# Performance work log

Hardware: AMD Instinct MI355X
Metric: run time of the kernel (lower is better)

## Reference

```python
import jax, jax.numpy as jnp
import numpy as np


def setup_inputs() -> dict:
    key = jax.random.key(0)
    ks = jax.random.split(key, 8)
    Na, Nb = 4096, 4096
    Fa, Fb, D = 512, 512, 128
    E = 131072  # avg degree 32
    x_a = jax.random.normal(ks[0], (Na, Fa), dtype=jnp.float32)
    x_b = jax.random.normal(ks[1], (Nb, Fb), dtype=jnp.float32)
    W_a = jax.random.normal(ks[2], (Fa, D), dtype=jnp.float32) / np.sqrt(Fa).astype(np.float32)
    b_a = jnp.zeros((D,), dtype=jnp.float32)
    W_b = jax.random.normal(ks[3], (Fb, D), dtype=jnp.float32) / np.sqrt(Fb).astype(np.float32)
    b_b = jnp.zeros((D,), dtype=jnp.float32)
    edge_index_ab = jax.random.randint(ks[4], (2, E), 0, Nb, dtype=jnp.int64)  # rows in [0,Na), cols in [0,Nb)
    edge_index_ba = jax.random.randint(ks[5], (2, E), 0, Na, dtype=jnp.int64)  # rows in [0,Nb), cols in [0,Na)
    return {"x_a": x_a, "x_b": x_b, "W_a": W_a, "b_a": b_a, "W_b": W_b, "b_b": b_b,
            "edge_index_ab": edge_index_ab, "edge_index_ba": edge_index_ba}


def reference(x_a, x_b, W_a, b_a, W_b, b_b, edge_index_ab, edge_index_ba):
    Na, Nb = x_a.shape[0], x_b.shape[0]
    dt = x_a.dtype
    # per-node-type feature projections (LATTE.feature_projection + relu activation)
    h_a = jax.nn.relu(x_a @ W_a + b_a)  # [Na, D]
    h_b = jax.nn.relu(x_b @ W_b + b_b)  # [Nb, D]
    # sparse adjacencies as dense scatters (edge values = 1.0, duplicates accumulate like coalesced SpGEMM)
    A = jnp.zeros((Na, Nb), dtype=dt).at[edge_index_ab[0], edge_index_ab[1]].add(1.0)
    B = jnp.zeros((Nb, Na), dtype=dt).at[edge_index_ba[0], edge_index_ba[1]].add(1.0)
    # adamic-adar degree normalization: deg_A = colcount(A), deg_B = rowcount(B), both over shared dim k=Nb
    deg_A = jnp.zeros((Nb,), dtype=dt).at[edge_index_ab[1]].add(1.0)
    deg_B = jnp.zeros((Nb,), dtype=dt).at[edge_index_ba[0]].add(1.0)
    deg = deg_A + deg_B
    d = jnp.where(deg > 0, 1.0 / jnp.maximum(deg, 1.0), 0.0)  # inf -> 0 as in original
    # out = A @ D @ B  (adamic-adar composed metapath adjacency)
    C = (A * d[None, :]) @ B  # [Na, Na]
    # metapath aggregation: 2nd-order (composed) path on h_a plus 1st-order neighbors of type b
    out = C @ h_a + A @ h_b  # [Na, D]
    return out
```

## Files before the change

kernel.cpp:

```cpp
#include <hip/hip_runtime.h>


#define D_FEAT 128
#define F_IN 512
#define BCAP 256
#define NROW 4096

using short8 = __attribute__((ext_vector_type(8))) short;
using ushort4v = __attribute__((ext_vector_type(4))) unsigned short;
using f32x4  = __attribute__((ext_vector_type(4))) float;

struct Params {
    const float* xa; const float* Wa; const float* ba;
    const float* xb; const float* Wb; const float* bb;
    const int* ab_row; const int* ab_col;
    const int* ba_row; const int* ba_col;
    short* WfA; short* WfB;
    unsigned short* ha_bf;
    float* hb;
    unsigned* u_bf;
    int* cnt_ab; int* cnt_ba; int* degc;
    unsigned short* buck_ab; unsigned short* buck_ba;
    float* out;
    int Eab; int Eba;
};

__device__ inline unsigned short f2bf(float f) {
    unsigned u = __builtin_bit_cast(unsigned, f);
    unsigned r = (u + 0x7FFFu + ((u >> 16) & 1u)) >> 16;
    return (unsigned short)r;
}
__device__ inline float bf2f(unsigned short s) {
    unsigned u = ((unsigned)s) << 16;
    return __builtin_bit_cast(float, u);
}

__global__ __launch_bounds__(256) void w_prep_k(Params P) {
    int g = blockIdx.x * 256 + threadIdx.x;
    for (int z = g; z < 3 * NROW; z += 16384) P.cnt_ab[z] = 0;
    const float* W = (g < 8192) ? P.Wa : P.Wb;
    short* Wf = (g < 8192) ? P.WfA : P.WfB;
    int i = g & 8191;
    int l = i & 63;
    int c = (i >> 6) & 7;
    int t = i >> 9;
    int col = c * 16 + (l & 15);
    int kbase = t * 32 + (l >> 4) * 8;
    short8 o;
#pragma unroll
    for (int e = 0; e < 8; ++e) o[e] = (short)f2bf(W[(size_t)(kbase + e) * D_FEAT + col]);
    *(short8*)(Wf + (size_t)i * 8) = o;
}

__global__ __launch_bounds__(256) void edges_gemm_k(Params P, int nblk_g) {
    int blk = blockIdx.x;
    if (blk >= nblk_g) {
        int base = (blk - nblk_g) * 512 + threadIdx.x;
#pragma unroll
        for (int q = 0; q < 2; ++q) {
            int g = base + q * 256;
            if (g < P.Eab) {
                int r = P.ab_row[g], c = P.ab_col[g];
                int p = atomicAdd(&P.cnt_ab[r], 1);
                if (p < BCAP) P.buck_ab[(size_t)r * BCAP + p] = (unsigned short)c;
                atomicAdd(&P.degc[c], 1);
            } else if (g < P.Eab + P.Eba) {
                int e = g - P.Eab;
                int r = P.ba_row[e], c = P.ba_col[e];
                int p = atomicAdd(&P.cnt_ba[r], 1);
                if (p < BCAP) P.buck_ba[(size_t)r * BCAP + p] = (unsigned short)c;
            }
        }
        return;
    }
    __shared__ float red[4][16][132];
    const int tid = threadIdx.x;
    const bool isA = (blk < 256);
    const float* x; const short* Wf; const float* bias;
    if (isA) { x = P.xa; Wf = P.WfA; bias = P.ba; }
    else { blk -= 256; x = P.xb; Wf = P.WfB; bias = P.bb; }
    const int row0 = blk * 16;
    const int w = tid >> 6;
    const int l = tid & 63;
    const int lr = l & 15;
    const int lk = l >> 4;

    f32x4 acc[8];
#pragma unroll
    for (int c = 0; c < 8; ++c) acc[c] = (f32x4){0.f, 0.f, 0.f, 0.f};

    const float* xrow = x + (size_t)(row0 + lr) * F_IN;
    float4 xf[8];
#pragma unroll
    for (int ks = 0; ks < 4; ++ks) {
        const int k0 = (w * 4 + ks) * 32 + lk * 8;
        xf[2 * ks]     = *(const float4*)(xrow + k0);
        xf[2 * ks + 1] = *(const float4*)(xrow + k0 + 4);
    }

#pragma unroll
    for (int ks = 0; ks < 4; ++ks) {
        const int t = w * 4 + ks;
        float4 xf0 = xf[2 * ks];
        float4 xf1 = xf[2 * ks + 1];
        short8 afr;
        afr[0] = (short)f2bf(xf0.x); afr[1] = (short)f2bf(xf0.y);
        afr[2] = (short)f2bf(xf0.z); afr[3] = (short)f2bf(xf0.w);
        afr[4] = (short)f2bf(xf1.x); afr[5] = (short)f2bf(xf1.y);
        afr[6] = (short)f2bf(xf1.z); afr[7] = (short)f2bf(xf1.w);
        const short8* wfp = (const short8*)Wf + ((size_t)t * 8 * 64 + l);
#pragma unroll
        for (int c = 0; c < 8; ++c) {
            short8 bfr = wfp[c * 64];
            acc[c] = __builtin_amdgcn_mfma_f32_16x16x32_bf16(afr, bfr, acc[c], 0, 0, 0);
        }
    }

#pragma unroll
    for (int c = 0; c < 8; ++c)
#pragma unroll
        for (int r = 0; r < 4; ++r)
            red[w][lk * 4 + r][c * 16 + lr] = acc[c][r];
    __syncthreads();

#pragma unroll
    for (int q = 0; q < 2; ++q) {
        int fi = tid * 2 + q;
        int r = fi >> 5;
        int c4 = fi & 31;
        float4 s0 = *(const float4*)&red[0][r][c4 * 4];
        float4 s1 = *(const float4*)&red[1][r][c4 * 4];
        float4 s2 = *(const float4*)&red[2][r][c4 * 4];
        float4 s3 = *(const float4*)&red[3][r][c4 * 4];
        float4 bv = ((const float4*)bias)[c4];
        float ox = fmaxf(s0.x + s1.x + s2.x + s3.x + bv.x, 0.0f);
        float oy = fmaxf(s0.y + s1.y + s2.y + s3.y + bv.y, 0.0f);
        float oz = fmaxf(s0.z + s1.z + s2.z + s3.z + bv.z, 0.0f);
        float ow = fmaxf(s0.w + s1.w + s2.w + s3.w + bv.w, 0.0f);
        if (isA) {
            ushort4v ob;
            ob[0] = f2bf(ox); ob[1] = f2bf(oy); ob[2] = f2bf(oz); ob[3] = f2bf(ow);
            *(ushort4v*)(P.ha_bf + (size_t)(row0 + r) * D_FEAT + c4 * 4) = ob;
        } else {
            float4 o; o.x = ox; o.y = oy; o.z = oz; o.w = ow;
            ((float4*)(P.hb + (size_t)(row0 + r) * D_FEAT))[c4] = o;
        }
    }
}

#define GATHER8(CBASE)                                                        \
    {                                                                         \
        int c0 = cols[CBASE],     c1 = cols[CBASE + 1];                       \
        int c2 = cols[CBASE + 2], c3 = cols[CBASE + 3];                       \
        int c4 = cols[CBASE + 4], c5 = cols[CBASE + 5];                       \
        int c6 = cols[CBASE + 6], c7 = cols[CBASE + 7];                       \
        unsigned v0 = s2[(size_t)c0 * 64 + lane];                             \
        unsigned v1 = s2[(size_t)c1 * 64 + lane];                             \
        unsigned v2 = s2[(size_t)c2 * 64 + lane];                             \
        unsigned v3 = s2[(size_t)c3 * 64 + lane];                             \
        unsigned v4 = s2[(size_t)c4 * 64 + lane];                             \
        unsigned v5 = s2[(size_t)c5 * 64 + lane];                             \
        unsigned v6 = s2[(size_t)c6 * 64 + lane];                             \
        unsigned v7 = s2[(size_t)c7 * 64 + lane];                             \
        ax += (bf2f((unsigned short)v0) + bf2f((unsigned short)v1)) +         \
              (bf2f((unsigned short)v2) + bf2f((unsigned short)v3)) +         \
              ((bf2f((unsigned short)v4) + bf2f((unsigned short)v5)) +        \
               (bf2f((unsigned short)v6) + bf2f((unsigned short)v7)));        \
        ay += (bf2f((unsigned short)(v0 >> 16)) + bf2f((unsigned short)(v1 >> 16))) + \
              (bf2f((unsigned short)(v2 >> 16)) + bf2f((unsigned short)(v3 >> 16))) + \
              ((bf2f((unsigned short)(v4 >> 16)) + bf2f((unsigned short)(v5 >> 16))) + \
               (bf2f((unsigned short)(v6 >> 16)) + bf2f((unsigned short)(v7 >> 16)))); \
    }

__global__ __launch_bounds__(256) void gather_u_k(Params P) {
    int r = blockIdx.x * 4 + (threadIdx.x >> 6);
    if (r >= NROW) return;
    int lane = threadIdx.x & 63;
    int ncb = P.cnt_ba[r];
    int dgc = P.degc[r];
    float2 hbv = ((const float2*)P.hb)[(size_t)r * 64 + lane];
    int n = ncb > BCAP ? BCAP : ncb;
    const unsigned short* cols = P.buck_ba + (size_t)r * BCAP;
    const unsigned* s2 = (const unsigned*)P.ha_bf;
    float ax = 0.0f, ay = 0.0f;
    int e = 0;
    for (; e + 15 < n; e += 16) { GATHER8(e) GATHER8(e + 8) }
    for (; e + 3 < n; e += 4) {
        int c0 = cols[e], c1 = cols[e + 1], c2 = cols[e + 2], c3 = cols[e + 3];
        unsigned v0 = s2[(size_t)c0 * 64 + lane];
        unsigned v1 = s2[(size_t)c1 * 64 + lane];
        unsigned v2 = s2[(size_t)c2 * 64 + lane];
        unsigned v3 = s2[(size_t)c3 * 64 + lane];
        ax += (bf2f((unsigned short)v0) + bf2f((unsigned short)v1)) +
              (bf2f((unsigned short)v2) + bf2f((unsigned short)v3));
        ay += (bf2f((unsigned short)(v0 >> 16)) + bf2f((unsigned short)(v1 >> 16))) +
              (bf2f((unsigned short)(v2 >> 16)) + bf2f((unsigned short)(v3 >> 16)));
    }
    for (; e < n; ++e) {
        unsigned v = s2[(size_t)cols[e] * 64 + lane];
        ax += bf2f((unsigned short)v);
        ay += bf2f((unsigned short)(v >> 16));
    }
    float dgf = (float)(dgc + ncb);
    float inv = dgf > 0.0f ? 1.0f / dgf : 0.0f;
    float ux = ax * inv + hbv.x;
    float uy = ay * inv + hbv.y;
    P.u_bf[(size_t)r * 64 + lane] = (unsigned)f2bf(ux) | ((unsigned)f2bf(uy) << 16);
}

__global__ __launch_bounds__(256) void gather_out_k(Params P) {
    int r = blockIdx.x * 4 + (threadIdx.x >> 6);
    if (r >= NROW) return;
    int lane = threadIdx.x & 63;
    int n = P.cnt_ab[r];
    if (n > BCAP) n = BCAP;
    const unsigned short* cols = P.buck_ab + (size_t)r * BCAP;
    const unsigned* s2 = P.u_bf;
    float ax = 0.0f, ay = 0.0f;
    int e = 0;
    for (; e + 15 < n; e += 16) { GATHER8(e) GATHER8(e + 8) }
    for (; e + 3 < n; e += 4) {
        int c0 = cols[e], c1 = cols[e + 1], c2 = cols[e + 2], c3 = cols[e + 3];
        unsigned v0 = s2[(size_t)c0 * 64 + lane];
        unsigned v1 = s2[(size_t)c1 * 64 + lane];
        unsigned v2 = s2[(size_t)c2 * 64 + lane];
        unsigned v3 = s2[(size_t)c3 * 64 + lane];
        ax += (bf2f((unsigned short)v0) + bf2f((unsigned short)v1)) +
              (bf2f((unsigned short)v2) + bf2f((unsigned short)v3));
        ay += (bf2f((unsigned short)(v0 >> 16)) + bf2f((unsigned short)(v1 >> 16))) +
              (bf2f((unsigned short)(v2 >> 16)) + bf2f((unsigned short)(v3 >> 16)));
    }
    for (; e < n; ++e) {
        unsigned v = s2[(size_t)cols[e] * 64 + lane];
        ax += bf2f((unsigned short)v);
        ay += bf2f((unsigned short)(v >> 16));
    }
    float2 o; o.x = ax; o.y = ay;
    ((float2*)P.out)[(size_t)r * 64 + lane] = o;
}

extern "C" void kernel_launch(void* const* d_in, const int* in_sizes, int n_in,
                              void* d_out, int out_size, void* d_ws, size_t ws_size,
                              hipStream_t stream) {
    const float* x_a = (const float*)d_in[0];
    const float* x_b = (const float*)d_in[1];
    const float* W_a = (const float*)d_in[2];
    const float* b_a = (const float*)d_in[3];
    const float* W_b = (const float*)d_in[4];
    const float* b_b = (const float*)d_in[5];
    const int* ei_ab = (const int*)d_in[6];
    const int* ei_ba = (const int*)d_in[7];

    const int D = in_sizes[3];
    const int Fa = in_sizes[2] / D;
    const int Na = in_sizes[0] / Fa;
    const int Fb = in_sizes[4] / D;
    const int Nb = in_sizes[1] / Fb;
    const int Eab = in_sizes[6] / 2;
    const int Eba = in_sizes[7] / 2;

    char* p = (char*)d_ws;
    unsigned short* ha_bf = (unsigned short*)p; p += (size_t)Na * D * 2;
    float* h_b = (float*)p; p += (size_t)Nb * D * 4;
    unsigned* u_bf = (unsigned*)p; p += (size_t)Nb * (D / 2) * 4;
    unsigned short* buck_ab = (unsigned short*)p; p += (size_t)Na * BCAP * 2;
    unsigned short* buck_ba = (unsigned short*)p; p += (size_t)Nb * BCAP * 2;
    short* WfA = (short*)p; p += (size_t)Fa * D * 2;
    short* WfB = (short*)p; p += (size_t)Fb * D * 2;
    int* cnt_ab = (int*)p; p += (size_t)Na * 4;
    int* cnt_ba = (int*)p; p += (size_t)Nb * 4;
    int* degc   = (int*)p; p += (size_t)Nb * 4;

    Params P;
    P.xa = x_a; P.Wa = W_a; P.ba = b_a;
    P.xb = x_b; P.Wb = W_b; P.bb = b_b;
    P.ab_row = ei_ab; P.ab_col = ei_ab + Eab;
    P.ba_row = ei_ba; P.ba_col = ei_ba + Eba;
    P.WfA = WfA; P.WfB = WfB;
    P.ha_bf = ha_bf; P.hb = h_b; P.u_bf = u_bf;
    P.cnt_ab = cnt_ab; P.cnt_ba = cnt_ba; P.degc = degc;
    P.buck_ab = buck_ab; P.buck_ba = buck_ba;
    P.out = (float*)d_out;
    P.Eab = Eab; P.Eba = Eba;

    w_prep_k<<<64, 256, 0, stream>>>(P);

    int nblk_g = Na / 16 + Nb / 16;
    int nEdgeBlk = (Eab + Eba + 511) / 512;
    edges_gemm_k<<<nblk_g + nEdgeBlk, 256, 0, stream>>>(P, nblk_g);

    gather_u_k<<<(Nb + 3) / 4, 256, 0, stream>>>(P);

    gather_out_k<<<(Na + 3) / 4, 256, 0, stream>>>(P);
}
```

Measured before the change: 46.70 us.

## Give each wave a full-K GEMM tile and store h_b as bf16

The projection GEMM used to split K across four waves and reduce the partial sums through shared memory with a barrier. Now each wave owns a 16-row tile and walks the whole K range itself, so the LDS reduction and __syncthreads go away, and the GEMM part shrinks from 512 blocks to 128. h_b is also stored as bf16 instead of fp32, halving its write and read traffic in the gather kernel at some precision cost. The trade-off is less parallelism per tile and a longer serial chain of MFMAs per wave, plus narrow scattered 2-byte stores in the epilogue.

```diff
diff --git a/kernel.cpp b/kernel.cpp
--- a/kernel.cpp
+++ b/kernel.cpp
@@ -5,9 +5,9 @@
 #define F_IN 512
 #define BCAP 256
 #define NROW 4096
+#define NGEMMBLK 128
 
 using short8 = __attribute__((ext_vector_type(8))) short;
-using ushort4v = __attribute__((ext_vector_type(4))) unsigned short;
 using f32x4  = __attribute__((ext_vector_type(4))) float;
 
 struct Params {
@@ -17,7 +17,7 @@
     const int* ba_row; const int* ba_col;
     short* WfA; short* WfB;
     unsigned short* ha_bf;
-    float* hb;
+    unsigned short* hb_bf;
     unsigned* u_bf;
     int* cnt_ab; int* cnt_ba; int* degc;
     unsigned short* buck_ab; unsigned short* buck_ba;
@@ -52,10 +52,10 @@
     *(short8*)(Wf + (size_t)i * 8) = o;
 }
 
-__global__ __launch_bounds__(256) void edges_gemm_k(Params P, int nblk_g) {
+__global__ __launch_bounds__(256) void edges_gemm_k(Params P) {
     int blk = blockIdx.x;
-    if (blk >= nblk_g) {
-        int base = (blk - nblk_g) * 512 + threadIdx.x;
+    if (blk >= NGEMMBLK) {
+        int base = (blk - NGEMMBLK) * 512 + threadIdx.x;
 #pragma unroll
         for (int q = 0; q < 2; ++q) {
             int g = base + q * 256;
@@ -73,15 +73,14 @@
         }
         return;
     }
-    __shared__ float red[4][16][132];
-    const int tid = threadIdx.x;
-    const bool isA = (blk < 256);
-    const float* x; const short* Wf; const float* bias;
-    if (isA) { x = P.xa; Wf = P.WfA; bias = P.ba; }
-    else { blk -= 256; x = P.xb; Wf = P.WfB; bias = P.bb; }
-    const int row0 = blk * 16;
-    const int w = tid >> 6;
-    const int l = tid & 63;
+    const int wid = blk * 4 + (threadIdx.x >> 6);
+    const int l = threadIdx.x & 63;
+    const bool isA = (wid < 256);
+    const float* x;  const short* Wf;  const float* bias;  unsigned short* h;
+    int tile;
+    if (isA) { x = P.xa; Wf = P.WfA; bias = P.ba; h = P.ha_bf; tile = wid; }
+    else     { x = P.xb; Wf = P.WfB; bias = P.bb; h = P.hb_bf; tile = wid - 256; }
+    const int row0 = tile * 16;
     const int lr = l & 15;
     const int lk = l >> 4;
 
@@ -89,20 +88,11 @@
 #pragma unroll
     for (int c = 0; c < 8; ++c) acc[c] = (f32x4){0.f, 0.f, 0.f, 0.f};
 
-    const float* xrow = x + (size_t)(row0 + lr) * F_IN;
-    float4 xf[8];
-#pragma unroll
-    for (int ks = 0; ks < 4; ++ks) {
-        const int k0 = (w * 4 + ks) * 32 + lk * 8;
-        xf[2 * ks]     = *(const float4*)(xrow + k0);
-        xf[2 * ks + 1] = *(const float4*)(xrow + k0 + 4);
-    }
-
-#pragma unroll
-    for (int ks = 0; ks < 4; ++ks) {
-        const int t = w * 4 + ks;
-        float4 xf0 = xf[2 * ks];
-        float4 xf1 = xf[2 * ks + 1];
+    const float* xrow = x + (size_t)(row0 + lr) * F_IN + lk * 8;
+#pragma unroll 4
+    for (int t = 0; t < 16; ++t) {
+        float4 xf0 = *(const float4*)(xrow + t * 32);
+        float4 xf1 = *(const float4*)(xrow + t * 32 + 4);
         short8 afr;
         afr[0] = (short)f2bf(xf0.x); afr[1] = (short)f2bf(xf0.y);
         afr[2] = (short)f2bf(xf0.z); afr[3] = (short)f2bf(xf0.w);
@@ -117,33 +107,12 @@
     }
 
 #pragma unroll
-    for (int c = 0; c < 8; ++c)
-#pragma unroll
-        for (int r = 0; r < 4; ++r)
-            red[w][lk * 4 + r][c * 16 + lr] = acc[c][r];
-    __syncthreads();
-
-#pragma unroll
-    for (int q = 0; q < 2; ++q) {
-        int fi = tid * 2 + q;
-        int r = fi >> 5;
-        int c4 = fi & 31;
-        float4 s0 = *(const float4*)&red[0][r][c4 * 4];
-        float4 s1 = *(const float4*)&red[1][r][c4 * 4];
-        float4 s2 = *(const float4*)&red[2][r][c4 * 4];
-        float4 s3 = *(const float4*)&red[3][r][c4 * 4];
-        float4 bv = ((const float4*)bias)[c4];
-        float ox = fmaxf(s0.x + s1.x + s2.x + s3.x + bv.x, 0.0f);
-        float oy = fmaxf(s0.y + s1.y + s2.y + s3.y + bv.y, 0.0f);
-        float oz = fmaxf(s0.z + s1.z + s2.z + s3.z + bv.z, 0.0f);
-        float ow = fmaxf(s0.w + s1.w + s2.w + s3.w + bv.w, 0.0f);
-        if (isA) {
-            ushort4v ob;
-            ob[0] = f2bf(ox); ob[1] = f2bf(oy); ob[2] = f2bf(oz); ob[3] = f2bf(ow);
-            *(ushort4v*)(P.ha_bf + (size_t)(row0 + r) * D_FEAT + c4 * 4) = ob;
-        } else {
-            float4 o; o.x = ox; o.y = oy; o.z = oz; o.w = ow;
-            ((float4*)(P.hb + (size_t)(row0 + r) * D_FEAT))[c4] = o;
+    for (int c = 0; c < 8; ++c) {
+        float bv = bias[c * 16 + lr];
+#pragma unroll
+        for (int r = 0; r < 4; ++r) {
+            float v = fmaxf(acc[c][r] + bv, 0.0f);
+            h[(size_t)(row0 + lk * 4 + r) * D_FEAT + c * 16 + lr] = f2bf(v);
         }
     }
 }
@@ -178,7 +147,7 @@
     int lane = threadIdx.x & 63;
     int ncb = P.cnt_ba[r];
     int dgc = P.degc[r];
-    float2 hbv = ((const float2*)P.hb)[(size_t)r * 64 + lane];
+    unsigned hbw = ((const unsigned*)P.hb_bf)[(size_t)r * 64 + lane];
     int n = ncb > BCAP ? BCAP : ncb;
     const unsigned short* cols = P.buck_ba + (size_t)r * BCAP;
     const unsigned* s2 = (const unsigned*)P.ha_bf;
@@ -203,8 +172,8 @@
     }
     float dgf = (float)(dgc + ncb);
     float inv = dgf > 0.0f ? 1.0f / dgf : 0.0f;
-    float ux = ax * inv + hbv.x;
-    float uy = ay * inv + hbv.y;
+    float ux = ax * inv + bf2f((unsigned short)hbw);
+    float uy = ay * inv + bf2f((unsigned short)(hbw >> 16));
     P.u_bf[(size_t)r * 64 + lane] = (unsigned)f2bf(ux) | ((unsigned)f2bf(uy) << 16);
 }
 
@@ -261,7 +230,7 @@
 
     char* p = (char*)d_ws;
     unsigned short* ha_bf = (unsigned short*)p; p += (size_t)Na * D * 2;
-    float* h_b = (float*)p; p += (size_t)Nb * D * 4;
+    unsigned short* hb_bf = (unsigned short*)p; p += (size_t)Nb * D * 2;
     unsigned* u_bf = (unsigned*)p; p += (size_t)Nb * (D / 2) * 4;
     unsigned short* buck_ab = (unsigned short*)p; p += (size_t)Na * BCAP * 2;
     unsigned short* buck_ba = (unsigned short*)p; p += (size_t)Nb * BCAP * 2;
@@ -277,7 +246,7 @@
     P.ab_row = ei_ab; P.ab_col = ei_ab + Eab;
     P.ba_row = ei_ba; P.ba_col = ei_ba + Eba;
     P.WfA = WfA; P.WfB = WfB;
-    P.ha_bf = ha_bf; P.hb = h_b; P.u_bf = u_bf;
+    P.ha_bf = ha_bf; P.hb_bf = hb_bf; P.u_bf = u_bf;
     P.cnt_ab = cnt_ab; P.cnt_ba = cnt_ba; P.degc = degc;
     P.buck_ab = buck_ab; P.buck_ba = buck_ba;
     P.out = (float*)d_out;
@@ -285,9 +254,8 @@
 
     w_prep_k<<<64, 256, 0, stream>>>(P);
 
-    int nblk_g = Na / 16 + Nb / 16;
     int nEdgeBlk = (Eab + Eba + 511) / 512;
-    edges_gemm_k<<<nblk_g + nEdgeBlk, 256, 0, stream>>>(P, nblk_g);
+    edges_gemm_k<<<NGEMMBLK + nEdgeBlk, 256, 0, stream>>>(P);
 
     gather_u_k<<<(Nb + 3) / 4, 256, 0, stream>>>(P);
 
```

Measured after the change: 76.60 us. 64.0% more time.
